# Kernel optimization log

Measured on AMD Instinct MI355X. Metric: run time of the kernel, lower is better.

Reference implementation:

```python
import jax, jax.numpy as jnp
import numpy as np

B, S, IN, OUT = 4, 2048, 4096, 4096


def setup_inputs() -> dict:
    key = jax.random.key(0)
    k1, k2 = jax.random.split(key, 2)
    x = jax.random.normal(k1, (B, S, IN), dtype=jnp.float32)
    # Materialize the quantized weight the way bitsandbytes int8_vectorwise_quant does:
    # per-output-row absmax (SCB) and int8 codes CB = round(W * 127 / absmax_row).
    Wf = jax.random.normal(k2, (OUT, IN), dtype=jnp.float32) * 0.02
    absmax = jnp.max(jnp.abs(Wf), axis=1)  # [OUT]
    CB = jnp.round(Wf * (127.0 / absmax)[:, None]).astype(jnp.int8)  # [OUT, IN]
    SCB = absmax.astype(jnp.float32)  # [OUT], per-row absmax scale
    return {"x": x, "CB": CB, "SCB": SCB}


def reference(x, CB, SCB):
    # LLM.int8()-style forward (has_fp16_weights=False, no outlier split needed for
    # well-behaved activations): dynamic row-wise int8 quantization of x, int8 GEMM
    # accumulated in int32, then dequant by (absmax_x/127) * (SCB/127).
    absmax_x = jnp.max(jnp.abs(x), axis=-1, keepdims=True)  # [B,S,1]
    sx = absmax_x / 127.0
    xq = jnp.round(x / sx).astype(jnp.int8)  # [B,S,IN]
    acc = jnp.einsum("bsk,ok->bso", xq, CB, preferred_element_type=jnp.int32)
    y = acc.astype(jnp.float32) * sx * (SCB / 127.0)[None, None, :]  # [B,S,OUT]
    return y
```

## Files before the change

### kernel.cpp

```cpp
#include <hip/hip_runtime.h>
#include <stdint.h>

static constexpr int Mtot = 8192;
static constexpr int Ntot = 4096;
static constexpr int Ktot = 4096;

using i32x4 = __attribute__((ext_vector_type(4))) int;

#define GLD16(gptr, lptr)                                                                   \
  __builtin_amdgcn_global_load_lds((const __attribute__((address_space(1))) void*)(gptr),   \
                                   (__attribute__((address_space(3))) void*)(lptr), 16, 0, 0)
#define WAITVM(N) asm volatile("s_waitcnt vmcnt(" #N ")" ::: "memory")

__global__ __launch_bounds__(256) void prep_kernel(const int* __restrict__ cb32,
                                                   int8_t* __restrict__ cb8,
                                                   const float* __restrict__ x,
                                                   int8_t* __restrict__ xq,
                                                   float* __restrict__ sx) {
  __shared__ float wmax[4];
  if (blockIdx.x < 16384) {
    const int idx = blockIdx.x * 256 + threadIdx.x;
    const int4 v = reinterpret_cast<const int4*>(cb32)[idx];
    const unsigned packed = (unsigned)(v.x & 0xff) | ((unsigned)(v.y & 0xff) << 8) |
                            ((unsigned)(v.z & 0xff) << 16) | ((unsigned)(v.w & 0xff) << 24);
    reinterpret_cast<unsigned*>(cb8)[idx] = packed;
    return;
  }
  const int row = blockIdx.x - 16384;
  const float4* xr = reinterpret_cast<const float4*>(x + (size_t)row * Ktot);
  float4 v[4];
  float am = 0.f;
#pragma unroll
  for (int i = 0; i < 4; ++i) {
    v[i] = xr[threadIdx.x + i * 256];
    am = fmaxf(am, fmaxf(fmaxf(fabsf(v[i].x), fabsf(v[i].y)),
                         fmaxf(fabsf(v[i].z), fabsf(v[i].w))));
  }
#pragma unroll
  for (int off = 32; off > 0; off >>= 1) am = fmaxf(am, __shfl_xor(am, off));
  if ((threadIdx.x & 63) == 0) wmax[threadIdx.x >> 6] = am;
  __syncthreads();
  am = fmaxf(fmaxf(wmax[0], wmax[1]), fmaxf(wmax[2], wmax[3]));
  const float inv = 127.0f / am;
  if (threadIdx.x == 0) sx[row] = am * (1.0f / 127.0f);
  unsigned* dq = reinterpret_cast<unsigned*>(xq + (size_t)row * Ktot);
#pragma unroll
  for (int i = 0; i < 4; ++i) {
    const int q0 = (int)rintf(v[i].x * inv);
    const int q1 = (int)rintf(v[i].y * inv);
    const int q2 = (int)rintf(v[i].z * inv);
    const int q3 = (int)rintf(v[i].w * inv);
    dq[threadIdx.x + i * 256] = (unsigned)(q0 & 0xff) | ((unsigned)(q1 & 0xff) << 8) |
                                ((unsigned)(q2 & 0xff) << 16) | ((unsigned)(q3 & 0xff) << 24);
  }
}

__global__ __launch_bounds__(512, 2) void gemm_i8_kernel(const int8_t* __restrict__ A,
                                                         const int8_t* __restrict__ B,
                                                         const float* __restrict__ sx,
                                                         const float* __restrict__ scb,
                                                         float* __restrict__ C) {
  constexpr int BK = 128;
  constexpr int NT = Ktot / BK;
  __shared__ __align__(16) int8_t lds[131072];

  const int tid = threadIdx.x;
  const int lane = tid & 63;
  const int wid = tid >> 6;

  const int wg = (int)blockIdx.x;
  const int wgs = (wg & 7) * 64 + (wg >> 3);
  const int m0 = (wgs >> 4) * 256;
  const int n0 = (wgs & 15) * 256;

  const int wm = (wid >> 2) * 128;
  const int wn = (wid & 3) * 64;

  const int srow = tid >> 3;
  const int scol = ((tid & 7) * 16) ^ ((srow & 7) << 4);
  const int8_t* gA = A + (size_t)(m0 + srow) * Ktot + scol;
  const int8_t* gB = B + (size_t)(n0 + srow) * Ktot + scol;

  const int l15 = lane & 15;
  const int lc0 = ((lane >> 4) * 16) ^ ((lane & 7) << 4);
  const int aOff = (wm + l15) * 128 + lc0;
  const int bOff = 65536 + (wn + l15) * 128 + lc0;

  i32x4 acc[8][4];
#pragma unroll
  for (int f = 0; f < 8; ++f)
#pragma unroll
    for (int g = 0; g < 4; ++g) acc[f][g] = (i32x4)0;

  i32x4 aE[4], aO[4], b0v[4], b1v[4];

#pragma unroll
  for (int i = 0; i < 4; ++i) GLD16(gB + (size_t)(i * 64) * Ktot, &lds[65536 + i * 8192 + tid * 16]);
  GLD16(gA + (size_t)(0 * 64) * Ktot, &lds[0 * 8192 + tid * 16]);
  GLD16(gA + (size_t)(2 * 64) * Ktot, &lds[2 * 8192 + tid * 16]);
  GLD16(gA + (size_t)(1 * 64) * Ktot, &lds[1 * 8192 + tid * 16]);
  GLD16(gA + (size_t)(3 * 64) * Ktot, &lds[3 * 8192 + tid * 16]);
  WAITVM(2);
  __builtin_amdgcn_s_barrier();
#pragma unroll
  for (int f = 0; f < 4; ++f) aE[f] = *(const i32x4*)&lds[aOff + f * 2048];
#pragma unroll
  for (int g = 0; g < 4; ++g) b0v[g] = *(const i32x4*)&lds[bOff + g * 2048];

#pragma unroll 2
  for (int t = 0; t < NT - 1; ++t) {
    const int bo = (t & 1) * 32768;
    const int so = bo ^ 32768;
    const size_t kn = (size_t)(t + 1) * BK;

#pragma unroll
    for (int f = 0; f < 4; ++f) aO[f] = *(const i32x4*)&lds[bo + (aOff ^ 64) + f * 2048];
#pragma unroll
    for (int g = 0; g < 4; ++g) b1v[g] = *(const i32x4*)&lds[bo + (bOff ^ 64) + g * 2048];
#pragma unroll
    for (int i = 0; i < 4; ++i)
      GLD16(gB + kn + (size_t)(i * 64) * Ktot, &lds[65536 + so + i * 8192 + tid * 16]);
    GLD16(gA + kn + (size_t)(0 * 64) * Ktot, &lds[so + 0 * 8192 + tid * 16]);
    GLD16(gA + kn + (size_t)(2 * 64) * Ktot, &lds[so + 2 * 8192 + tid * 16]);
    GLD16(gA + kn + (size_t)(1 * 64) * Ktot, &lds[so + 1 * 8192 + tid * 16]);
    GLD16(gA + kn + (size_t)(3 * 64) * Ktot, &lds[so + 3 * 8192 + tid * 16]);
    __builtin_amdgcn_s_setprio(1);
#pragma unroll
    for (int f = 0; f < 4; ++f)
#pragma unroll
      for (int g = 0; g < 4; ++g)
        acc[f][g] = __builtin_amdgcn_mfma_i32_16x16x64_i8(aE[f], b0v[g], acc[f][g], 0, 0, 0);
    __builtin_amdgcn_s_setprio(0);
    WAITVM(8);
    __builtin_amdgcn_s_barrier();

#pragma unroll
    for (int f = 0; f < 4; ++f) aE[f] = *(const i32x4*)&lds[bo + aOff + (f + 4) * 2048];
    __builtin_amdgcn_s_setprio(1);
#pragma unroll
    for (int f = 0; f < 4; ++f)
#pragma unroll
      for (int g = 0; g < 4; ++g)
        acc[f][g] = __builtin_amdgcn_mfma_i32_16x16x64_i8(aO[f], b1v[g], acc[f][g], 0, 0, 0);
    __builtin_amdgcn_s_setprio(0);

#pragma unroll
    for (int f = 0; f < 4; ++f) aO[f] = *(const i32x4*)&lds[bo + (aOff ^ 64) + (f + 4) * 2048];
    __builtin_amdgcn_s_setprio(1);
#pragma unroll
    for (int f = 0; f < 4; ++f)
#pragma unroll
      for (int g = 0; g < 4; ++g)
        acc[f + 4][g] = __builtin_amdgcn_mfma_i32_16x16x64_i8(aE[f], b0v[g], acc[f + 4][g], 0, 0, 0);
    __builtin_amdgcn_s_setprio(0);
    WAITVM(2);
    __builtin_amdgcn_s_barrier();

#pragma unroll
    for (int f = 0; f < 4; ++f) aE[f] = *(const i32x4*)&lds[so + aOff + f * 2048];
#pragma unroll
    for (int g = 0; g < 4; ++g) b0v[g] = *(const i32x4*)&lds[so + bOff + g * 2048];
    __builtin_amdgcn_s_setprio(1);
#pragma unroll
    for (int f = 0; f < 4; ++f)
#pragma unroll
      for (int g = 0; g < 4; ++g)
        acc[f + 4][g] = __builtin_amdgcn_mfma_i32_16x16x64_i8(aO[f], b1v[g], acc[f + 4][g], 0, 0, 0);
    __builtin_amdgcn_s_setprio(0);
  }

  {
    const int bo = ((NT - 1) & 1) * 32768;
#pragma unroll
    for (int f = 0; f < 4; ++f) aO[f] = *(const i32x4*)&lds[bo + (aOff ^ 64) + f * 2048];
#pragma unroll
    for (int g = 0; g < 4; ++g) b1v[g] = *(const i32x4*)&lds[bo + (bOff ^ 64) + g * 2048];
    __builtin_amdgcn_s_setprio(1);
#pragma unroll
    for (int f = 0; f < 4; ++f)
#pragma unroll
      for (int g = 0; g < 4; ++g)
        acc[f][g] = __builtin_amdgcn_mfma_i32_16x16x64_i8(aE[f], b0v[g], acc[f][g], 0, 0, 0);
    __builtin_amdgcn_s_setprio(0);
    WAITVM(0);
    __builtin_amdgcn_s_barrier();
#pragma unroll
    for (int f = 0; f < 4; ++f) aE[f] = *(const i32x4*)&lds[bo + aOff + (f + 4) * 2048];
    __builtin_amdgcn_s_setprio(1);
#pragma unroll
    for (int f = 0; f < 4; ++f)
#pragma unroll
      for (int g = 0; g < 4; ++g)
        acc[f][g] = __builtin_amdgcn_mfma_i32_16x16x64_i8(aO[f], b1v[g], acc[f][g], 0, 0, 0);
    __builtin_amdgcn_s_setprio(0);
#pragma unroll
    for (int f = 0; f < 4; ++f) aO[f] = *(const i32x4*)&lds[bo + (aOff ^ 64) + (f + 4) * 2048];
    __builtin_amdgcn_s_setprio(1);
#pragma unroll
    for (int f = 0; f < 4; ++f)
#pragma unroll
      for (int g = 0; g < 4; ++g)
        acc[f + 4][g] = __builtin_amdgcn_mfma_i32_16x16x64_i8(aE[f], b0v[g], acc[f + 4][g], 0, 0, 0);
    __builtin_amdgcn_s_setprio(0);
    __builtin_amdgcn_s_setprio(1);
#pragma unroll
    for (int f = 0; f < 4; ++f)
#pragma unroll
      for (int g = 0; g < 4; ++g)
        acc[f + 4][g] = __builtin_amdgcn_mfma_i32_16x16x64_i8(aO[f], b1v[g], acc[f + 4][g], 0, 0, 0);
    __builtin_amdgcn_s_setprio(0);
  }

  const int col = lane & 15;
  const int rbase = (lane >> 4) * 4;
#pragma unroll
  for (int f = 0; f < 8; ++f) {
    const int gmb = m0 + wm + f * 16 + rbase;
    float sm[4];
#pragma unroll
    for (int r = 0; r < 4; ++r) sm[r] = sx[gmb + r];
#pragma unroll
    for (int g = 0; g < 4; ++g) {
      const int gn = n0 + wn + g * 16 + col;
      const float snv = scb[gn] * (1.0f / 127.0f);
#pragma unroll
      for (int r = 0; r < 4; ++r)
        C[(size_t)(gmb + r) * Ntot + gn] = (float)acc[f][g][r] * sm[r] * snv;
    }
  }
}

extern "C" void kernel_launch(void* const* d_in, const int* in_sizes, int n_in,
                              void* d_out, int out_size, void* d_ws, size_t ws_size,
                              hipStream_t stream) {
  const float* x = (const float*)d_in[0];
  const int* CB32 = (const int*)d_in[1];
  const float* SCB = (const float*)d_in[2];
  float* out = (float*)d_out;

  int8_t* xq = (int8_t*)d_ws;
  int8_t* cb8 = (int8_t*)d_ws + (size_t)Mtot * Ktot;
  float* sx = (float*)((int8_t*)d_ws + (size_t)Mtot * Ktot + (size_t)Ntot * Ktot);

  prep_kernel<<<16384 + Mtot, 256, 0, stream>>>(CB32, cb8, x, xq, sx);
  gemm_i8_kernel<<<512, 512, 0, stream>>>(xq, cb8, sx, SCB, out);
}
```

Baseline: 376.3 us.

## Switch int8 GEMM inner product from 16x16x64 to 32x32x32 MFMA tiles

Replaces the 16x16x64 int8 MFMA fragments with 32x32x32 MFMA instructions, reorganising per-wave register fragments (4x2 tiles of 32x32 accumulators), LDS read offsets with the existing XOR swizzle, and the epilogue row mapping. Larger MFMA tiles raise operand reuse per LDS read and reduce the number of LDS loads and MFMA issues per unit of work. In exchange, the 32x32 instructions have longer latency and different register pressure, and the epilogue stores follow a new row layout that may coalesce differently.

```diff
diff --git a/kernel.cpp b/kernel.cpp
--- a/kernel.cpp
+++ b/kernel.cpp
@@ -6,11 +6,13 @@
 static constexpr int Ktot = 4096;
 
 using i32x4 = __attribute__((ext_vector_type(4))) int;
+using i32x16 = __attribute__((ext_vector_type(16))) int;
 
 #define GLD16(gptr, lptr)                                                                   \
   __builtin_amdgcn_global_load_lds((const __attribute__((address_space(1))) void*)(gptr),   \
                                    (__attribute__((address_space(3))) void*)(lptr), 16, 0, 0)
 #define WAITVM(N) asm volatile("s_waitcnt vmcnt(" #N ")" ::: "memory")
+#define MFMA32(a, b, c) __builtin_amdgcn_mfma_i32_32x32x32_i8((a), (b), (c), 0, 0, 0)
 
 __global__ __launch_bounds__(256) void prep_kernel(const int* __restrict__ cb32,
                                                    int8_t* __restrict__ cb8,
@@ -81,18 +83,23 @@
   const int8_t* gA = A + (size_t)(m0 + srow) * Ktot + scol;
   const int8_t* gB = B + (size_t)(n0 + srow) * Ktot + scol;
 
-  const int l15 = lane & 15;
-  const int lc0 = ((lane >> 4) * 16) ^ ((lane & 7) << 4);
-  const int aOff = (wm + l15) * 128 + lc0;
-  const int bOff = 65536 + (wn + l15) * 128 + lc0;
-
-  i32x4 acc[8][4];
-#pragma unroll
-  for (int f = 0; f < 8; ++f)
-#pragma unroll
-    for (int g = 0; g < 4; ++g) acc[f][g] = (i32x4)0;
-
-  i32x4 aE[4], aO[4], b0v[4], b1v[4];
+  const int l31 = lane & 31;
+  const int lcA = ((lane >> 5) * 16) ^ ((lane & 7) << 4);
+  const int kc0 = lcA, kc1 = lcA ^ 32, kc2 = lcA ^ 64, kc3 = lcA ^ 96;
+  const int aR0 = (wm + 0 * 32 + l31) * 128;
+  const int aR1 = (wm + 1 * 32 + l31) * 128;
+  const int aR2 = (wm + 2 * 32 + l31) * 128;
+  const int aR3 = (wm + 3 * 32 + l31) * 128;
+  const int bR0 = 65536 + (wn + 0 * 32 + l31) * 128;
+  const int bR1 = 65536 + (wn + 1 * 32 + l31) * 128;
+
+  i32x16 acc[4][2];
+#pragma unroll
+  for (int f = 0; f < 4; ++f)
+#pragma unroll
+    for (int g = 0; g < 2; ++g) acc[f][g] = (i32x16)0;
+
+  i32x4 aC[4], aN[4], bLo[4], bHi[4];
 
 #pragma unroll
   for (int i = 0; i < 4; ++i) GLD16(gB + (size_t)(i * 64) * Ktot, &lds[65536 + i * 8192 + tid * 16]);
@@ -102,10 +109,14 @@
   GLD16(gA + (size_t)(3 * 64) * Ktot, &lds[3 * 8192 + tid * 16]);
   WAITVM(2);
   __builtin_amdgcn_s_barrier();
-#pragma unroll
-  for (int f = 0; f < 4; ++f) aE[f] = *(const i32x4*)&lds[aOff + f * 2048];
-#pragma unroll
-  for (int g = 0; g < 4; ++g) b0v[g] = *(const i32x4*)&lds[bOff + g * 2048];
+  aC[0] = *(const i32x4*)&lds[aR0 + kc0];
+  aC[1] = *(const i32x4*)&lds[aR0 + kc1];
+  aC[2] = *(const i32x4*)&lds[aR1 + kc0];
+  aC[3] = *(const i32x4*)&lds[aR1 + kc1];
+  bLo[0] = *(const i32x4*)&lds[bR0 + kc0];
+  bLo[1] = *(const i32x4*)&lds[bR0 + kc1];
+  bLo[2] = *(const i32x4*)&lds[bR1 + kc0];
+  bLo[3] = *(const i32x4*)&lds[bR1 + kc1];
 
 #pragma unroll 2
   for (int t = 0; t < NT - 1; ++t) {
@@ -113,10 +124,14 @@
     const int so = bo ^ 32768;
     const size_t kn = (size_t)(t + 1) * BK;
 
-#pragma unroll
-    for (int f = 0; f < 4; ++f) aO[f] = *(const i32x4*)&lds[bo + (aOff ^ 64) + f * 2048];
-#pragma unroll
-    for (int g = 0; g < 4; ++g) b1v[g] = *(const i32x4*)&lds[bo + (bOff ^ 64) + g * 2048];
+    aN[0] = *(const i32x4*)&lds[bo + aR0 + kc2];
+    aN[1] = *(const i32x4*)&lds[bo + aR0 + kc3];
+    aN[2] = *(const i32x4*)&lds[bo + aR1 + kc2];
+    aN[3] = *(const i32x4*)&lds[bo + aR1 + kc3];
+    bHi[0] = *(const i32x4*)&lds[bo + bR0 + kc2];
+    bHi[1] = *(const i32x4*)&lds[bo + bR0 + kc3];
+    bHi[2] = *(const i32x4*)&lds[bo + bR1 + kc2];
+    bHi[3] = *(const i32x4*)&lds[bo + bR1 + kc3];
 #pragma unroll
     for (int i = 0; i < 4; ++i)
       GLD16(gB + kn + (size_t)(i * 64) * Ktot, &lds[65536 + so + i * 8192 + tid * 16]);
@@ -125,107 +140,153 @@
     GLD16(gA + kn + (size_t)(1 * 64) * Ktot, &lds[so + 1 * 8192 + tid * 16]);
     GLD16(gA + kn + (size_t)(3 * 64) * Ktot, &lds[so + 3 * 8192 + tid * 16]);
     __builtin_amdgcn_s_setprio(1);
-#pragma unroll
-    for (int f = 0; f < 4; ++f)
-#pragma unroll
-      for (int g = 0; g < 4; ++g)
-        acc[f][g] = __builtin_amdgcn_mfma_i32_16x16x64_i8(aE[f], b0v[g], acc[f][g], 0, 0, 0);
+    acc[0][0] = MFMA32(aC[0], bLo[0], acc[0][0]);
+    acc[0][0] = MFMA32(aC[1], bLo[1], acc[0][0]);
+    acc[0][1] = MFMA32(aC[0], bLo[2], acc[0][1]);
+    acc[0][1] = MFMA32(aC[1], bLo[3], acc[0][1]);
+    acc[1][0] = MFMA32(aC[2], bLo[0], acc[1][0]);
+    acc[1][0] = MFMA32(aC[3], bLo[1], acc[1][0]);
+    acc[1][1] = MFMA32(aC[2], bLo[2], acc[1][1]);
+    acc[1][1] = MFMA32(aC[3], bLo[3], acc[1][1]);
     __builtin_amdgcn_s_setprio(0);
     WAITVM(8);
     __builtin_amdgcn_s_barrier();
 
-#pragma unroll
-    for (int f = 0; f < 4; ++f) aE[f] = *(const i32x4*)&lds[bo + aOff + (f + 4) * 2048];
-    __builtin_amdgcn_s_setprio(1);
-#pragma unroll
-    for (int f = 0; f < 4; ++f)
-#pragma unroll
-      for (int g = 0; g < 4; ++g)
-        acc[f][g] = __builtin_amdgcn_mfma_i32_16x16x64_i8(aO[f], b1v[g], acc[f][g], 0, 0, 0);
-    __builtin_amdgcn_s_setprio(0);
-
-#pragma unroll
-    for (int f = 0; f < 4; ++f) aO[f] = *(const i32x4*)&lds[bo + (aOff ^ 64) + (f + 4) * 2048];
-    __builtin_amdgcn_s_setprio(1);
-#pragma unroll
-    for (int f = 0; f < 4; ++f)
-#pragma unroll
-      for (int g = 0; g < 4; ++g)
-        acc[f + 4][g] = __builtin_amdgcn_mfma_i32_16x16x64_i8(aE[f], b0v[g], acc[f + 4][g], 0, 0, 0);
+    aC[0] = *(const i32x4*)&lds[bo + aR2 + kc0];
+    aC[1] = *(const i32x4*)&lds[bo + aR2 + kc1];
+    aC[2] = *(const i32x4*)&lds[bo + aR3 + kc0];
+    aC[3] = *(const i32x4*)&lds[bo + aR3 + kc1];
+    __builtin_amdgcn_s_setprio(1);
+    acc[0][0] = MFMA32(aN[0], bHi[0], acc[0][0]);
+    acc[0][0] = MFMA32(aN[1], bHi[1], acc[0][0]);
+    acc[0][1] = MFMA32(aN[0], bHi[2], acc[0][1]);
+    acc[0][1] = MFMA32(aN[1], bHi[3], acc[0][1]);
+    acc[1][0] = MFMA32(aN[2], bHi[0], acc[1][0]);
+    acc[1][0] = MFMA32(aN[3], bHi[1], acc[1][0]);
+    acc[1][1] = MFMA32(aN[2], bHi[2], acc[1][1]);
+    acc[1][1] = MFMA32(aN[3], bHi[3], acc[1][1]);
+    __builtin_amdgcn_s_setprio(0);
+
+    aN[0] = *(const i32x4*)&lds[bo + aR2 + kc2];
+    aN[1] = *(const i32x4*)&lds[bo + aR2 + kc3];
+    aN[2] = *(const i32x4*)&lds[bo + aR3 + kc2];
+    aN[3] = *(const i32x4*)&lds[bo + aR3 + kc3];
+    __builtin_amdgcn_s_setprio(1);
+    acc[2][0] = MFMA32(aC[0], bLo[0], acc[2][0]);
+    acc[2][0] = MFMA32(aC[1], bLo[1], acc[2][0]);
+    acc[2][1] = MFMA32(aC[0], bLo[2], acc[2][1]);
+    acc[2][1] = MFMA32(aC[1], bLo[3], acc[2][1]);
+    acc[3][0] = MFMA32(aC[2], bLo[0], acc[3][0]);
+    acc[3][0] = MFMA32(aC[3], bLo[1], acc[3][0]);
+    acc[3][1] = MFMA32(aC[2], bLo[2], acc[3][1]);
+    acc[3][1] = MFMA32(aC[3], bLo[3], acc[3][1]);
     __builtin_amdgcn_s_setprio(0);
     WAITVM(2);
     __builtin_amdgcn_s_barrier();
 
-#pragma unroll
-    for (int f = 0; f < 4; ++f) aE[f] = *(const i32x4*)&lds[so + aOff + f * 2048];
-#pragma unroll
-    for (int g = 0; g < 4; ++g) b0v[g] = *(const i32x4*)&lds[so + bOff + g * 2048];
-    __builtin_amdgcn_s_setprio(1);
-#pragma unroll
-    for (int f = 0; f < 4; ++f)
-#pragma unroll
-      for (int g = 0; g < 4; ++g)
-        acc[f + 4][g] = __builtin_amdgcn_mfma_i32_16x16x64_i8(aO[f], b1v[g], acc[f + 4][g], 0, 0, 0);
+    aC[0] = *(const i32x4*)&lds[so + aR0 + kc0];
+    aC[1] = *(const i32x4*)&lds[so + aR0 + kc1];
+    aC[2] = *(const i32x4*)&lds[so + aR1 + kc0];
+    aC[3] = *(const i32x4*)&lds[so + aR1 + kc1];
+    bLo[0] = *(const i32x4*)&lds[so + bR0 + kc0];
+    bLo[1] = *(const i32x4*)&lds[so + bR0 + kc1];
+    bLo[2] = *(const i32x4*)&lds[so + bR1 + kc0];
+    bLo[3] = *(const i32x4*)&lds[so + bR1 + kc1];
+    __builtin_amdgcn_s_setprio(1);
+    acc[2][0] = MFMA32(aN[0], bHi[0], acc[2][0]);
+    acc[2][0] = MFMA32(aN[1], bHi[1], acc[2][0]);
+    acc[2][1] = MFMA32(aN[0], bHi[2], acc[2][1]);
+    acc[2][1] = MFMA32(aN[1], bHi[3], acc[2][1]);
+    acc[3][0] = MFMA32(aN[2], bHi[0], acc[3][0]);
+    acc[3][0] = MFMA32(aN[3], bHi[1], acc[3][0]);
+    acc[3][1] = MFMA32(aN[2], bHi[2], acc[3][1]);
+    acc[3][1] = MFMA32(aN[3], bHi[3], acc[3][1]);
     __builtin_amdgcn_s_setprio(0);
   }
 
   {
     const int bo = ((NT - 1) & 1) * 32768;
-#pragma unroll
-    for (int f = 0; f < 4; ++f) aO[f] = *(const i32x4*)&lds[bo + (aOff ^ 64) + f * 2048];
-#pragma unroll
-    for (int g = 0; g < 4; ++g) b1v[g] = *(const i32x4*)&lds[bo + (bOff ^ 64) + g * 2048];
-    __builtin_amdgcn_s_setprio(1);
-#pragma unroll
-    for (int f = 0; f < 4; ++f)
-#pragma unroll
-      for (int g = 0; g < 4; ++g)
-        acc[f][g] = __builtin_amdgcn_mfma_i32_16x16x64_i8(aE[f], b0v[g], acc[f][g], 0, 0, 0);
+    aN[0] = *(const i32x4*)&lds[bo + aR0 + kc2];
+    aN[1] = *(const i32x4*)&lds[bo + aR0 + kc3];
+    aN[2] = *(const i32x4*)&lds[bo + aR1 + kc2];
+    aN[3] = *(const i32x4*)&lds[bo + aR1 + kc3];
+    bHi[0] = *(const i32x4*)&lds[bo + bR0 + kc2];
+    bHi[1] = *(const i32x4*)&lds[bo + bR0 + kc3];
+    bHi[2] = *(const i32x4*)&lds[bo + bR1 + kc2];
+    bHi[3] = *(const i32x4*)&lds[bo + bR1 + kc3];
+    __builtin_amdgcn_s_setprio(1);
+    acc[0][0] = MFMA32(aC[0], bLo[0], acc[0][0]);
+    acc[0][0] = MFMA32(aC[1], bLo[1], acc[0][0]);
+    acc[0][1] = MFMA32(aC[0], bLo[2], acc[0][1]);
+    acc[0][1] = MFMA32(aC[1], bLo[3], acc[0][1]);
+    acc[1][0] = MFMA32(aC[2], bLo[0], acc[1][0]);
+    acc[1][0] = MFMA32(aC[3], bLo[1], acc[1][0]);
+    acc[1][1] = MFMA32(aC[2], bLo[2], acc[1][1]);
+    acc[1][1] = MFMA32(aC[3], bLo[3], acc[1][1]);
     __builtin_amdgcn_s_setprio(0);
     WAITVM(0);
     __builtin_amdgcn_s_barrier();
-#pragma unroll
-    for (int f = 0; f < 4; ++f) aE[f] = *(const i32x4*)&lds[bo + aOff + (f + 4) * 2048];
-    __builtin_amdgcn_s_setprio(1);
-#pragma unroll
-    for (int f = 0; f < 4; ++f)
-#pragma unroll
-      for (int g = 0; g < 4; ++g)
-        acc[f][g] = __builtin_amdgcn_mfma_i32_16x16x64_i8(aO[f], b1v[g], acc[f][g], 0, 0, 0);
-    __builtin_amdgcn_s_setprio(0);
-#pragma unroll
-    for (int f = 0; f < 4; ++f) aO[f] = *(const i32x4*)&lds[bo + (aOff ^ 64) + (f + 4) * 2048];
-    __builtin_amdgcn_s_setprio(1);
-#pragma unroll
-    for (int f = 0; f < 4; ++f)
-#pragma unroll
-      for (int g = 0; g < 4; ++g)
-        acc[f + 4][g] = __builtin_amdgcn_mfma_i32_16x16x64_i8(aE[f], b0v[g], acc[f + 4][g], 0, 0, 0);
-    __builtin_amdgcn_s_setprio(0);
-    __builtin_amdgcn_s_setprio(1);
-#pragma unroll
-    for (int f = 0; f < 4; ++f)
-#pragma unroll
-      for (int g = 0; g < 4; ++g)
-        acc[f + 4][g] = __builtin_amdgcn_mfma_i32_16x16x64_i8(aO[f], b1v[g], acc[f + 4][g], 0, 0, 0);
-    __builtin_amdgcn_s_setprio(0);
-  }
-
-  const int col = lane & 15;
-  const int rbase = (lane >> 4) * 4;
-#pragma unroll
-  for (int f = 0; f < 8; ++f) {
-    const int gmb = m0 + wm + f * 16 + rbase;
-    float sm[4];
-#pragma unroll
-    for (int r = 0; r < 4; ++r) sm[r] = sx[gmb + r];
-#pragma unroll
-    for (int g = 0; g < 4; ++g) {
-      const int gn = n0 + wn + g * 16 + col;
+    aC[0] = *(const i32x4*)&lds[bo + aR2 + kc0];
+    aC[1] = *(const i32x4*)&lds[bo + aR2 + kc1];
+    aC[2] = *(const i32x4*)&lds[bo + aR3 + kc0];
+    aC[3] = *(const i32x4*)&lds[bo + aR3 + kc1];
+    __builtin_amdgcn_s_setprio(1);
+    acc[0][0] = MFMA32(aN[0], bHi[0], acc[0][0]);
+    acc[0][0] = MFMA32(aN[1], bHi[1], acc[0][0]);
+    acc[0][1] = MFMA32(aN[0], bHi[2], acc[0][1]);
+    acc[0][1] = MFMA32(aN[1], bHi[3], acc[0][1]);
+    acc[1][0] = MFMA32(aN[2], bHi[0], acc[1][0]);
+    acc[1][0] = MFMA32(aN[3], bHi[1], acc[1][0]);
+    acc[1][1] = MFMA32(aN[2], bHi[2], acc[1][1]);
+    acc[1][1] = MFMA32(aN[3], bHi[3], acc[1][1]);
+    __builtin_amdgcn_s_setprio(0);
+    aN[0] = *(const i32x4*)&lds[bo + aR2 + kc2];
+    aN[1] = *(const i32x4*)&lds[bo + aR2 + kc3];
+    aN[2] = *(const i32x4*)&lds[bo + aR3 + kc2];
+    aN[3] = *(const i32x4*)&lds[bo + aR3 + kc3];
+    __builtin_amdgcn_s_setprio(1);
+    acc[2][0] = MFMA32(aC[0], bLo[0], acc[2][0]);
+    acc[2][0] = MFMA32(aC[1], bLo[1], acc[2][0]);
+    acc[2][1] = MFMA32(aC[0], bLo[2], acc[2][1]);
+    acc[2][1] = MFMA32(aC[1], bLo[3], acc[2][1]);
+    acc[3][0] = MFMA32(aC[2], bLo[0], acc[3][0]);
+    acc[3][0] = MFMA32(aC[3], bLo[1], acc[3][0]);
+    acc[3][1] = MFMA32(aC[2], bLo[2], acc[3][1]);
+    acc[3][1] = MFMA32(aC[3], bLo[3], acc[3][1]);
+    __builtin_amdgcn_s_setprio(0);
+    __builtin_amdgcn_s_setprio(1);
+    acc[2][0] = MFMA32(aN[0], bHi[0], acc[2][0]);
+    acc[2][0] = MFMA32(aN[1], bHi[1], acc[2][0]);
+    acc[2][1] = MFMA32(aN[0], bHi[2], acc[2][1]);
+    acc[2][1] = MFMA32(aN[1], bHi[3], acc[2][1]);
+    acc[3][0] = MFMA32(aN[2], bHi[0], acc[3][0]);
+    acc[3][0] = MFMA32(aN[3], bHi[1], acc[3][0]);
+    acc[3][1] = MFMA32(aN[2], bHi[2], acc[3][1]);
+    acc[3][1] = MFMA32(aN[3], bHi[3], acc[3][1]);
+    __builtin_amdgcn_s_setprio(0);
+  }
+
+  const int col = l31;
+  const int hi4 = (lane >> 5) * 4;
+#pragma unroll
+  for (int f = 0; f < 4; ++f) {
+    const int gmb = m0 + wm + f * 32;
+    float sm[16];
+#pragma unroll
+    for (int q = 0; q < 4; ++q)
+#pragma unroll
+      for (int r = 0; r < 4; ++r) sm[q * 4 + r] = sx[gmb + r + 8 * q + hi4];
+#pragma unroll
+    for (int g = 0; g < 2; ++g) {
+      const int gn = n0 + wn + g * 32 + col;
       const float snv = scb[gn] * (1.0f / 127.0f);
 #pragma unroll
-      for (int r = 0; r < 4; ++r)
-        C[(size_t)(gmb + r) * Ntot + gn] = (float)acc[f][g][r] * sm[r] * snv;
+      for (int q = 0; q < 4; ++q)
+#pragma unroll
+        for (int r = 0; r < 4; ++r) {
+          const int row = r + 8 * q + hi4;
+          C[(size_t)(gmb + row) * Ntot + gn] = (float)acc[f][g][q * 4 + r] * sm[q * 4 + r] * snv;
+        }
     }
   }
 }
```

Result: slower. 386.0 us (+2.6%).
